# Kernel tuning notes

Measured on AMD Instinct MI355X. Metric: run time of the kernel, lower is better.

The kernel has to match this reference:

```python
import jax, jax.numpy as jnp
import numpy as np

MIN_SIZE = 16.0
PH, PW, SCALE = 7, 7, 0.0625


def _context_anchor(rois, hh, hw):
    """rois: [N,5] (batch_idx,x1,y1,x2,y2). Returns [N*8,5] context boxes, col0 = 0 label."""
    N = rois.shape[0]
    x1, y1, x2, y2 = rois[:, 1], rois[:, 2], rois[:, 3], rois[:, 4]
    w, h = x2 - x1, y2 - y1
    k = jnp.arange(3, dtype=rois.dtype)
    sx = x1[:, None] + w[:, None] * (k - 0.5)  # x1 - w + w*k + w/2
    sy = y1[:, None] + h[:, None] * (k - 0.5)
    # np.meshgrid(shift_x, shift_y).ravel() is y-major
    cx = jnp.broadcast_to(sx[:, None, :], (N, 3, 3)).reshape(N, 9)
    cy = jnp.broadcast_to(sy[:, :, None], (N, 3, 3)).reshape(N, 9)
    boxes = jnp.stack([cx - w[:, None] / 4, cy - h[:, None] / 4,
                       cx + w[:, None] / 4, cy + h[:, None] / 4], -1)  # [N,9,4]
    bw = boxes[..., 2] - boxes[..., 0] + 1
    bh = boxes[..., 3] - boxes[..., 1] + 1
    invalid = ((boxes[..., 0] < 0) | (boxes[..., 1] < 0) |
               (boxes[..., 2] >= hw) | (boxes[..., 3] >= hh) |
               (bw < MIN_SIZE) | (bh < MIN_SIZE))
    boxes = jnp.where(invalid[..., None], rois[:, None, 1:5], boxes)
    boxes = boxes[:, jnp.array([0, 1, 2, 3, 5, 6, 7, 8]), :]  # drop center cell
    gt = boxes.reshape(N * 8, 4)  # K = 8N
    # IoU(all roi boxes, gt) with +1 pixel convention (bbox_overlaps_batch)
    A = rois[:, 1:5]
    aw, ah = A[:, 2] - A[:, 0] + 1, A[:, 3] - A[:, 1] + 1
    gw, gh = gt[:, 2] - gt[:, 0] + 1, gt[:, 3] - gt[:, 1] + 1
    iw = jnp.maximum(jnp.minimum(A[:, None, 2], gt[None, :, 2]) - jnp.maximum(A[:, None, 0], gt[None, :, 0]) + 1, 0)
    ih = jnp.maximum(jnp.minimum(A[:, None, 3], gt[None, :, 3]) - jnp.maximum(A[:, None, 1], gt[None, :, 1]) + 1, 0)
    inter = iw * ih
    ov = inter / ((aw * ah)[:, None] + (gw * gh)[None, :] - inter)  # [N,K]
    ov = jnp.where(((gw == 1) & (gh == 1))[None, :], 0.0, ov)
    ov = jnp.where(((aw == 1) & (ah == 1))[:, None], -1.0, ov)
    gt_max = ov.max(0)          # best overlap per gt box
    best = ov.argmax(0)         # index of best-matching roi (torch's `_`)
    labels = gt_max >= 0.3
    w_cell, h_cell = gt[:, 2] - gt[:, 0], gt[:, 3] - gt[:, 1]
    rw = jnp.where(labels, rois[best, 3] - rois[best, 1], 0.0)
    rh = jnp.where(labels, rois[best, 4] - rois[best, 2], 0.0)
    labels = (labels & ~(jnp.maximum(rw, rh) >= jnp.maximum(w_cell, h_cell))
                     & ~(jnp.minimum(rw, rh) < jnp.minimum(w_cell, h_cell) / 3))
    gt = jnp.where(labels[:, None], rois[best][:, 1:5], gt)
    # original zeroes labels at the end -> label column is all zeros
    return jnp.concatenate([jnp.zeros((N * 8, 1), rois.dtype), gt], -1)


def _roi_pool(features, boxes, ph, pw, scale):
    """Classic Caffe max RoIPool. Assumes batch_size==1 (all batch indices 0)."""
    _, C, H, W = features.shape
    f = features[0]  # [C,H,W]
    sw = jnp.round(boxes[:, 1] * scale)
    sh = jnp.round(boxes[:, 2] * scale)
    ew = jnp.round(boxes[:, 3] * scale)
    eh = jnp.round(boxes[:, 4] * scale)
    bsh = jnp.maximum(eh - sh + 1, 1.0) / ph
    bsw = jnp.maximum(ew - sw + 1, 1.0) / pw
    ii = jnp.arange(ph, dtype=f.dtype)
    jj = jnp.arange(pw, dtype=f.dtype)
    hs = jnp.clip(jnp.floor(ii[None, :] * bsh[:, None]) + sh[:, None], 0, H)   # [R,ph]
    he = jnp.clip(jnp.ceil((ii[None, :] + 1) * bsh[:, None]) + sh[:, None], 0, H)
    ws = jnp.clip(jnp.floor(jj[None, :] * bsw[:, None]) + sw[:, None], 0, W)   # [R,pw]
    we = jnp.clip(jnp.ceil((jj[None, :] + 1) * bsw[:, None]) + sw[:, None], 0, W)
    hidx = jnp.arange(H, dtype=f.dtype)
    widx = jnp.arange(W, dtype=f.dtype)
    mask_h = (hidx >= hs[..., None]) & (hidx < he[..., None])  # [R,ph,H]
    mask_w = (widx >= ws[..., None]) & (widx < we[..., None])  # [R,pw,W]
    NEG = jnp.asarray(-1e30, f.dtype)
    # separable masked max: reduce W per pw-bin, then H per ph-bin
    colmax = jnp.stack([jnp.where(mask_w[:, j, None, None, :], f[None], NEG).max(-1)
                        for j in range(pw)], axis=1)           # [R,pw,C,H]
    out = jnp.stack([jnp.where(mask_h[:, i, None, None, :], colmax, NEG).max(-1)
                     for i in range(ph)], axis=1)              # [R,ph,pw,C]
    valid = mask_h.any(-1)[:, :, None] & mask_w.any(-1)[:, None, :]
    out = jnp.where(valid[..., None], out, 0.0)                # empty bins -> 0
    return jnp.transpose(out, (0, 3, 1, 2))                    # [R,C,ph,pw]


def reference(features, rois, hh, hw):
    N = rois.shape[0]
    gt = _context_anchor(rois, hh, hw).reshape(N, 8, 5)
    cat_rois = jnp.concatenate([rois[:, None, :], gt], 1).reshape(-1, 5)  # [9N,5]
    pool = _roi_pool(features, cat_rois, PH, PW, SCALE)                   # [9N,C,7,7]
    pool_feat = pool.reshape(N, -1, PW, PH)                               # [N,9C,7,7]
    return pool_feat, cat_rois


def setup_inputs() -> dict:
    key = jax.random.key(0)
    k1, k2, k3, k4, k5 = jax.random.split(key, 5)
    N, C, Hf, Wf, IMG = 32, 256, 40, 40, 640
    x1 = jax.random.uniform(k1, (N,), minval=0.0, maxval=IMG - 220.0)
    y1 = jax.random.uniform(k2, (N,), minval=0.0, maxval=IMG - 220.0)
    bw = jax.random.uniform(k3, (N,), minval=80.0, maxval=200.0)
    bh = jax.random.uniform(k4, (N,), minval=80.0, maxval=200.0)
    rois = jnp.stack([jnp.zeros((N,)), x1, y1, x1 + bw, y1 + bh], -1).astype(jnp.float32)
    features = jax.random.normal(k5, (1, C, Hf, Wf), dtype=jnp.float32)
    return {"features": features, "rois": rois, "hh": 640, "hw": 640}
```

## Files before the change

### kernel.cpp

```cpp
#include <hip/hip_runtime.h>
#include <math.h>

#define N_ROIS   32
#define N_CAT    (N_ROIS * 9)
#define C_FEAT   256
#define H_FEAT   40
#define W_FEAT   40
#define P_FEAT   (H_FEAT * W_FEAT)
#define PH       7
#define PW       7
#define SCALE    0.0625f
#define MIN_SIZE 16.0f
#define CELLS    (PH * PW)
#define POOL_PER_BOX (C_FEAT * CELLS)
#define OUT_POOL_ELEMS ((size_t)N_CAT * POOL_PER_BOX)

#define N_TRANS_BLOCKS (P_FEAT / 32 * (C_FEAT / 32))

#define CH_G     64
#define NCHG     4
#define NBLK     (N_CAT * NCHG)
#define TPB      448
#define WROWS    14
#define WCOLS    14
#define PIX      (WROWS * WCOLS)
#define SLOTS    (PIX + 2)
#define WIN_FLTS (SLOTS * CH_G)
#define OBUF_FLTS (CH_G * CELLS)
#define QPP      (CH_G / 4)
#define STAGE_N  (PIX * QPP)

__global__ void prep_kernel(const float* __restrict__ f,
                            const float* __restrict__ rois,
                            const int* __restrict__ hh_p,
                            const int* __restrict__ hw_p,
                            float* __restrict__ ft,
                            float* __restrict__ cat_out,
                            int use_transpose) {
    __shared__ float tile[32][33];
    __shared__ float R[N_ROIS * 5];
    const int bid = blockIdx.x;
    const int tid = threadIdx.x;

    if (bid < N_TRANS_BLOCKS) {
        if (!use_transpose) return;
        const int pt = (bid % (P_FEAT / 32)) * 32;
        const int ct = (bid / (P_FEAT / 32)) * 32;
        const int lx = tid & 31;
        const int ly = tid >> 5;
        #pragma unroll
        for (int i = 0; i < 32; i += 8)
            tile[ly + i][lx] = f[(ct + ly + i) * P_FEAT + (pt + lx)];
        __syncthreads();
        #pragma unroll
        for (int i = 0; i < 32; i += 8)
            ft[(pt + ly + i) * C_FEAT + (ct + lx)] = tile[lx][ly + i];
        return;
    }

    if (tid < N_ROIS * 5) R[tid] = rois[tid];
    __syncthreads();

    const float hh = (float)(*hh_p);
    const float hw = (float)(*hw_p);

    const int g = tid;
    const int n = g >> 3;
    const int j = g & 7;
    const int m = (j < 4) ? j : j + 1;
    const int r  = m / 3;
    const int cc = m % 3;

    const float x1 = R[n * 5 + 1], y1 = R[n * 5 + 2];
    const float x2 = R[n * 5 + 3], y2 = R[n * 5 + 4];
    const float w = x2 - x1, h = y2 - y1;

    const float cx = x1 + w * ((float)cc - 0.5f);
    const float cy = y1 + h * ((float)r  - 0.5f);
    float bx1 = cx - w * 0.25f;
    float by1 = cy - h * 0.25f;
    float bx2 = cx + w * 0.25f;
    float by2 = cy + h * 0.25f;
    const float bw = bx2 - bx1 + 1.0f;
    const float bh = by2 - by1 + 1.0f;
    const bool invalid = (bx1 < 0.0f) || (by1 < 0.0f) ||
                         (bx2 >= hw) || (by2 >= hh) ||
                         (bw < MIN_SIZE) || (bh < MIN_SIZE);
    if (invalid) { bx1 = x1; by1 = y1; bx2 = x2; by2 = y2; }

    const float gw = bx2 - bx1 + 1.0f;
    const float gh = by2 - by1 + 1.0f;
    const float garea = gw * gh;
    const bool gdeg = (gw == 1.0f) && (gh == 1.0f);

    float best_ov = -INFINITY;
    int best = 0;
    for (int a = 0; a < N_ROIS; ++a) {
        const float ax1 = R[a * 5 + 1], ay1 = R[a * 5 + 2];
        const float ax2 = R[a * 5 + 3], ay2 = R[a * 5 + 4];
        const float aw = ax2 - ax1 + 1.0f, ah = ay2 - ay1 + 1.0f;
        float iw = fminf(ax2, bx2) - fmaxf(ax1, bx1) + 1.0f;
        float ih = fminf(ay2, by2) - fmaxf(ay1, by1) + 1.0f;
        iw = fmaxf(iw, 0.0f);
        ih = fmaxf(ih, 0.0f);
        const float inter = iw * ih;
        float ov = inter / (aw * ah + garea - inter);
        if (gdeg) ov = 0.0f;
        if (aw == 1.0f && ah == 1.0f) ov = -1.0f;
        if (ov > best_ov) { best_ov = ov; best = a; }
    }

    bool label = (best_ov >= 0.3f);
    const float w_cell = bx2 - bx1;
    const float h_cell = by2 - by1;
    const float rw = label ? (R[best * 5 + 3] - R[best * 5 + 1]) : 0.0f;
    const float rh = label ? (R[best * 5 + 4] - R[best * 5 + 2]) : 0.0f;
    label = label &&
            !(fmaxf(rw, rh) >= fmaxf(w_cell, h_cell)) &&
            !(fminf(rw, rh) < fminf(w_cell, h_cell) / 3.0f);
    if (label) {
        bx1 = R[best * 5 + 1]; by1 = R[best * 5 + 2];
        bx2 = R[best * 5 + 3]; by2 = R[best * 5 + 4];
    }

    float* row = cat_out + (size_t)(n * 9 + 1 + j) * 5;
    row[0] = 0.0f;
    row[1] = bx1; row[2] = by1; row[3] = bx2; row[4] = by2;
    if (j == 0) {
        float* rr = cat_out + (size_t)(n * 9) * 5;
        #pragma unroll
        for (int t = 0; t < 5; ++t) rr[t] = R[n * 5 + t];
    }
}

__global__ __launch_bounds__(TPB) void
pool_v8(const float* __restrict__ ft,
        const float* __restrict__ cat_rois,
        float* __restrict__ out) {
    __shared__ __align__(16) float win[WIN_FLTS];

    const int s   = (blockIdx.x & 7) * (NBLK / 8) + (blockIdx.x >> 3);
    const int b   = s >> 2;
    const int cg  = s & 3;
    const int tid = threadIdx.x;
    const int cl  = tid & 63;
    const int i   = tid >> 6;

    const float* cr = cat_rois + (size_t)b * 5;
    const float bx1 = cr[1], by1 = cr[2], bx2 = cr[3], by2 = cr[4];
    const float sw = rintf(bx1 * SCALE);
    const float sh = rintf(by1 * SCALE);
    const float ew = rintf(bx2 * SCALE);
    const float eh = rintf(by2 * SCALE);
    const float bsh = fmaxf(eh - sh + 1.0f, 1.0f) * (1.0f / (float)PH);
    const float bsw = fmaxf(ew - sw + 1.0f, 1.0f) * (1.0f / (float)PW);

    const int hs = __builtin_amdgcn_readfirstlane(
        (int)fminf(fmaxf(floorf((float)i * bsh) + sh, 0.0f), (float)H_FEAT));
    const int he = __builtin_amdgcn_readfirstlane(
        (int)fminf(fmaxf(ceilf((float)(i + 1) * bsh) + sh, 0.0f), (float)H_FEAT));

    int ws[PW], we[PW];
    #pragma unroll
    for (int j = 0; j < PW; ++j) {
        ws[j] = __builtin_amdgcn_readfirstlane(
            (int)fminf(fmaxf(floorf((float)j * bsw) + sw, 0.0f), (float)W_FEAT));
        we[j] = __builtin_amdgcn_readfirstlane(
            (int)fminf(fmaxf(ceilf((float)(j + 1) * bsw) + sw, 0.0f), (float)W_FEAT));
    }
    const int xs = ws[0];
    const int ys = __builtin_amdgcn_readfirstlane(
        (int)fminf(fmaxf(sh, 0.0f), (float)H_FEAT));

    const bool narrow = (bsw <= 2.0f) && (bsh <= 2.0f);
    const bool rowv = (he > hs);

    if (narrow) {
        const float* fb = ft + cg * CH_G;
        #pragma unroll
        for (int t = 0; t < STAGE_N / TPB; ++t) {
            const int e = tid + t * TPB;
            const int q = e & (QPP - 1);
            const int p = e >> 4;
            const int py = p / WCOLS;
            const int px = p - py * WCOLS;
            const int gy = (ys + py < H_FEAT - 1) ? (ys + py) : (H_FEAT - 1);
            const int gx = (xs + px < W_FEAT - 1) ? (xs + px) : (W_FEAT - 1);
            const float4 v = *(const float4*)(fb + ((size_t)(gy * W_FEAT + gx)
                                                    << 8) + (q << 2));
            *(float4*)(win + p * CH_G + q * 4) = v;
        }
        __syncthreads();

        float mx[PW];
        #pragma unroll
        for (int j = 0; j < PW; ++j) mx[j] = -1e30f;

        int off[PW], nj[PW];
        #pragma unroll
        for (int j = 0; j < PW; ++j) {
            off[j] = ws[j] - xs;
            nj[j]  = we[j] - ws[j];
        }
        for (int y = hs; y < he; ++y) {
            const float* wr = win + (y - ys) * (WCOLS * CH_G) + cl;
            #pragma unroll
            for (int j = 0; j < PW; ++j) {
                const float* p0 = wr + off[j] * CH_G;
                const float d0 = p0[0];
                const float d1 = p0[CH_G];
                const float d2 = p0[2 * CH_G];
                if (nj[j] > 0) mx[j] = fmaxf(mx[j], d0);
                if (nj[j] > 1) mx[j] = fmaxf(mx[j], d1);
                if (nj[j] > 2) mx[j] = fmaxf(mx[j], d2);
            }
        }
        __syncthreads();

        float* orow = win + cl * CELLS + i * PW;
        #pragma unroll
        for (int j = 0; j < PW; ++j)
            orow[j] = (rowv && (nj[j] > 0)) ? mx[j] : 0.0f;
        __syncthreads();

        const float4* src = (const float4*)win;
        float4* dst = (float4*)(out + (size_t)b * POOL_PER_BOX
                                    + (size_t)cg * OBUF_FLTS);
        dst[tid] = src[tid];
        const int e2 = tid + TPB;
        if (e2 < OBUF_FLTS / 4) dst[e2] = src[e2];
    } else {
        const int c = cg * CH_G + cl;
        float mx[PW];
        #pragma unroll
        for (int j = 0; j < PW; ++j) mx[j] = -1e30f;
        for (int y = hs; y < he; ++y) {
            #pragma unroll
            for (int j = 0; j < PW; ++j)
                for (int x = ws[j]; x < we[j]; ++x)
                    mx[j] = fmaxf(mx[j], ft[(size_t)(y * W_FEAT + x) * C_FEAT + c]);
        }
        float* ob = out + (size_t)b * POOL_PER_BOX + (size_t)c * CELLS + i * PW;
        #pragma unroll
        for (int j = 0; j < PW; ++j)
            ob[j] = (rowv && (we[j] > ws[j])) ? mx[j] : 0.0f;
    }
}

__global__ __launch_bounds__(256) void
roi_pool_kernel_nchw(const float* __restrict__ feat,
                     const float* __restrict__ cat_rois,
                     float* __restrict__ out) {
    const int i = blockIdx.x / N_CAT;
    const int b = blockIdx.x % N_CAT;
    const int c = threadIdx.x;

    const float* cr = cat_rois + (size_t)b * 5;
    const float sw = rintf(cr[1] * SCALE);
    const float sh = rintf(cr[2] * SCALE);
    const float ew = rintf(cr[3] * SCALE);
    const float eh = rintf(cr[4] * SCALE);
    const float bsh = fmaxf(eh - sh + 1.0f, 1.0f) * (1.0f / (float)PH);
    const float bsw = fmaxf(ew - sw + 1.0f, 1.0f) * (1.0f / (float)PW);

    const int hs = (int)fminf(fmaxf(floorf((float)i * bsh) + sh, 0.0f), (float)H_FEAT);
    const int he = (int)fminf(fmaxf(ceilf((float)(i + 1) * bsh) + sh, 0.0f), (float)H_FEAT);
    int ws[PW], we[PW];
    #pragma unroll
    for (int j = 0; j < PW; ++j) {
        ws[j] = (int)fminf(fmaxf(floorf((float)j * bsw) + sw, 0.0f), (float)W_FEAT);
        we[j] = (int)fminf(fmaxf(ceilf((float)(j + 1) * bsw) + sw, 0.0f), (float)W_FEAT);
    }
    float mx[PW];
    #pragma unroll
    for (int j = 0; j < PW; ++j) mx[j] = -1e30f;
    for (int y = hs; y < he; ++y) {
        const float* fr = feat + (size_t)c * P_FEAT + y * W_FEAT;
        #pragma unroll
        for (int j = 0; j < PW; ++j)
            for (int x = ws[j]; x < we[j]; ++x)
                mx[j] = fmaxf(mx[j], fr[x]);
    }
    const bool rowv = (he > hs);
    float* ob = out + (size_t)b * POOL_PER_BOX + (size_t)c * CELLS + i * PW;
    #pragma unroll
    for (int j = 0; j < PW; ++j)
        ob[j] = (rowv && (we[j] > ws[j])) ? mx[j] : 0.0f;
}

extern "C" void kernel_launch(void* const* d_in, const int* in_sizes, int n_in,
                              void* d_out, int out_size, void* d_ws, size_t ws_size,
                              hipStream_t stream) {
    const float* features = (const float*)d_in[0];
    const float* rois     = (const float*)d_in[1];
    const int*   hh_p     = (const int*)d_in[2];
    const int*   hw_p     = (const int*)d_in[3];

    float* out      = (float*)d_out;
    float* cat_out  = out + OUT_POOL_ELEMS;
    float* ft       = (float*)d_ws;

    const size_t ft_bytes = (size_t)C_FEAT * P_FEAT * sizeof(float);
    const int use_transpose = (ws_size >= ft_bytes) ? 1 : 0;

    hipLaunchKernelGGL(prep_kernel, dim3(N_TRANS_BLOCKS + 1), dim3(256), 0, stream,
                       features, rois, hh_p, hw_p, ft, cat_out, use_transpose);

    if (use_transpose) {
        hipLaunchKernelGGL(pool_v8, dim3(NBLK), dim3(TPB), 0, stream,
                           ft, cat_out, out);
    } else {
        hipLaunchKernelGGL(roi_pool_kernel_nchw, dim3(PH * N_CAT), dim3(C_FEAT), 0, stream,
                           features, cat_out, out);
    }
}
```

Measured before the change: 79.59 us.

## Fuse prep and pooling into one cooperative kernel with atomic work queue

```diff
diff --git a/kernel.cpp b/kernel.cpp
--- a/kernel.cpp
+++ b/kernel.cpp
@@ -1,4 +1,5 @@
 #include <hip/hip_runtime.h>
+#include <hip/hip_cooperative_groups.h>
 #include <math.h>
 
 #define N_ROIS   32
@@ -19,7 +20,8 @@
 
 #define CH_G     64
 #define NCHG     4
-#define NBLK     (N_CAT * NCHG)
+#define NUNIT    (N_CAT * NCHG)
+#define NBLK8    1152
 #define TPB      448
 #define WROWS    14
 #define WCOLS    14
@@ -28,7 +30,246 @@
 #define WIN_FLTS (SLOTS * CH_G)
 #define OBUF_FLTS (CH_G * CELLS)
 #define QPP      (CH_G / 4)
-#define STAGE_N  (PIX * QPP)
+
+#define CBLK     384
+
+__global__ __launch_bounds__(TPB, 4) void
+coop_v9(const float* __restrict__ f,
+        const float* __restrict__ rois,
+        const int* __restrict__ hh_p,
+        const int* __restrict__ hw_p,
+        float* __restrict__ out,
+        float* __restrict__ ft) {
+    __shared__ __align__(16) float win[WIN_FLTS];
+    __shared__ unsigned su;
+
+    const int bid = blockIdx.x;
+    const int tid = threadIdx.x;
+    unsigned* ctr = (unsigned*)(ft + (size_t)C_FEAT * P_FEAT);
+    float* cat_out = out + OUT_POOL_ELEMS;
+
+    if (bid == 0 && tid == 0) atomicExch(ctr, 0u);
+
+    float (*tile)[33] = (float(*)[33])win;
+    #pragma unroll
+    for (int pass = 0; pass < 2; ++pass) {
+        const int tno = bid + pass * CBLK;
+        const bool act = (tno < N_TRANS_BLOCKS) && (pass == 0 || bid < N_TRANS_BLOCKS - CBLK);
+        if (!act) continue;
+        const int pt = (tno % (P_FEAT / 32)) * 32;
+        const int ct = (tno / (P_FEAT / 32)) * 32;
+        const int lx = tid & 31;
+        const int ly = (tid >> 5) & 7;
+        if (tid < 256) {
+            #pragma unroll
+            for (int ii = 0; ii < 32; ii += 8)
+                tile[ly + ii][lx] = f[(ct + ly + ii) * P_FEAT + (pt + lx)];
+        }
+        __syncthreads();
+        if (tid < 256) {
+            #pragma unroll
+            for (int ii = 0; ii < 32; ii += 8)
+                ft[(pt + ly + ii) * C_FEAT + (ct + lx)] = tile[lx][ly + ii];
+        }
+        __syncthreads();
+    }
+
+    if (bid == CBLK - 1) {
+        float* R = win;
+        if (tid < N_ROIS * 5) R[tid] = rois[tid];
+        __syncthreads();
+        if (tid < 256) {
+            const float hh = (float)(*hh_p);
+            const float hw = (float)(*hw_p);
+            const int g = tid;
+            const int n = g >> 3;
+            const int j = g & 7;
+            const int m = (j < 4) ? j : j + 1;
+            const int r  = m / 3;
+            const int cc = m % 3;
+
+            const float x1 = R[n * 5 + 1], y1 = R[n * 5 + 2];
+            const float x2 = R[n * 5 + 3], y2 = R[n * 5 + 4];
+            const float w = x2 - x1, h = y2 - y1;
+
+            const float cx = x1 + w * ((float)cc - 0.5f);
+            const float cy = y1 + h * ((float)r  - 0.5f);
+            float bx1 = cx - w * 0.25f;
+            float by1 = cy - h * 0.25f;
+            float bx2 = cx + w * 0.25f;
+            float by2 = cy + h * 0.25f;
+            const float bw = bx2 - bx1 + 1.0f;
+            const float bh = by2 - by1 + 1.0f;
+            const bool invalid = (bx1 < 0.0f) || (by1 < 0.0f) ||
+                                 (bx2 >= hw) || (by2 >= hh) ||
+                                 (bw < MIN_SIZE) || (bh < MIN_SIZE);
+            if (invalid) { bx1 = x1; by1 = y1; bx2 = x2; by2 = y2; }
+
+            const float gw = bx2 - bx1 + 1.0f;
+            const float gh = by2 - by1 + 1.0f;
+            const float garea = gw * gh;
+            const bool gdeg = (gw == 1.0f) && (gh == 1.0f);
+
+            float best_ov = -INFINITY;
+            int best = 0;
+            for (int a = 0; a < N_ROIS; ++a) {
+                const float ax1 = R[a * 5 + 1], ay1 = R[a * 5 + 2];
+                const float ax2 = R[a * 5 + 3], ay2 = R[a * 5 + 4];
+                const float aw = ax2 - ax1 + 1.0f, ah = ay2 - ay1 + 1.0f;
+                float iw = fminf(ax2, bx2) - fmaxf(ax1, bx1) + 1.0f;
+                float ih = fminf(ay2, by2) - fmaxf(ay1, by1) + 1.0f;
+                iw = fmaxf(iw, 0.0f);
+                ih = fmaxf(ih, 0.0f);
+                const float inter = iw * ih;
+                float ov = inter / (aw * ah + garea - inter);
+                if (gdeg) ov = 0.0f;
+                if (aw == 1.0f && ah == 1.0f) ov = -1.0f;
+                if (ov > best_ov) { best_ov = ov; best = a; }
+            }
+
+            bool label = (best_ov >= 0.3f);
+            const float w_cell = bx2 - bx1;
+            const float h_cell = by2 - by1;
+            const float rw = label ? (R[best * 5 + 3] - R[best * 5 + 1]) : 0.0f;
+            const float rh = label ? (R[best * 5 + 4] - R[best * 5 + 2]) : 0.0f;
+            label = label &&
+                    !(fmaxf(rw, rh) >= fmaxf(w_cell, h_cell)) &&
+                    !(fminf(rw, rh) < fminf(w_cell, h_cell) / 3.0f);
+            if (label) {
+                bx1 = R[best * 5 + 1]; by1 = R[best * 5 + 2];
+                bx2 = R[best * 5 + 3]; by2 = R[best * 5 + 4];
+            }
+
+            float* row = cat_out + (size_t)(n * 9 + 1 + j) * 5;
+            row[0] = 0.0f;
+            row[1] = bx1; row[2] = by1; row[3] = bx2; row[4] = by2;
+            if (j == 0) {
+                float* rr = cat_out + (size_t)(n * 9) * 5;
+                #pragma unroll
+                for (int t = 0; t < 5; ++t) rr[t] = R[n * 5 + t];
+            }
+        }
+        __syncthreads();
+    }
+
+    cooperative_groups::this_grid().sync();
+
+    const int cl = tid & 63;
+    const int i  = tid >> 6;
+
+    for (;;) {
+        if (tid == 0) su = atomicAdd(ctr, 1u);
+        __syncthreads();
+        const unsigned u = su;
+        if (u >= (unsigned)NUNIT) break;
+
+        const int b  = (int)(u >> 2);
+        const int cg = (int)(u & 3);
+
+        const float* cr = cat_out + (size_t)b * 5;
+        const float bx1 = cr[1], by1 = cr[2], bx2 = cr[3], by2 = cr[4];
+        const float sw = rintf(bx1 * SCALE);
+        const float sh = rintf(by1 * SCALE);
+        const float ew = rintf(bx2 * SCALE);
+        const float eh = rintf(by2 * SCALE);
+        const float bsh = fmaxf(eh - sh + 1.0f, 1.0f) * (1.0f / (float)PH);
+        const float bsw = fmaxf(ew - sw + 1.0f, 1.0f) * (1.0f / (float)PW);
+
+        const int hs = __builtin_amdgcn_readfirstlane(
+            (int)fminf(fmaxf(floorf((float)i * bsh) + sh, 0.0f), (float)H_FEAT));
+        const int he = __builtin_amdgcn_readfirstlane(
+            (int)fminf(fmaxf(ceilf((float)(i + 1) * bsh) + sh, 0.0f), (float)H_FEAT));
+
+        int ws[PW], we[PW];
+        #pragma unroll
+        for (int j = 0; j < PW; ++j) {
+            ws[j] = __builtin_amdgcn_readfirstlane(
+                (int)fminf(fmaxf(floorf((float)j * bsw) + sw, 0.0f), (float)W_FEAT));
+            we[j] = __builtin_amdgcn_readfirstlane(
+                (int)fminf(fmaxf(ceilf((float)(j + 1) * bsw) + sw, 0.0f), (float)W_FEAT));
+        }
+        const int xs = ws[0];
+        const int ys = __builtin_amdgcn_readfirstlane(
+            (int)fminf(fmaxf(sh, 0.0f), (float)H_FEAT));
+        const int yend = __builtin_amdgcn_readfirstlane(
+            (int)fminf(fmaxf(ceilf((float)PH * bsh) + sh, 0.0f), (float)H_FEAT));
+        const int WH = yend - ys;
+
+        const bool narrow = (bsw <= 2.0f) && (bsh <= 2.0f);
+        const bool rowv = (he > hs);
+
+        if (narrow) {
+            const float* fb = ft + cg * CH_G;
+            const int nq4 = WH * WCOLS * QPP;
+            for (int e = tid; e < nq4; e += TPB) {
+                const int q = e & (QPP - 1);
+                const int p = e >> 4;
+                const int py = p / WCOLS;
+                const int px = p - py * WCOLS;
+                const int gy = (ys + py < H_FEAT - 1) ? (ys + py) : (H_FEAT - 1);
+                const int gx = (xs + px < W_FEAT - 1) ? (xs + px) : (W_FEAT - 1);
+                const float4 v = *(const float4*)(fb + ((size_t)(gy * W_FEAT + gx)
+                                                        << 8) + (q << 2));
+                *(float4*)(win + p * CH_G + q * 4) = v;
+            }
+            __syncthreads();
+
+            float mx[PW];
+            #pragma unroll
+            for (int j = 0; j < PW; ++j) mx[j] = -1e30f;
+
+            int off[PW], nj[PW];
+            #pragma unroll
+            for (int j = 0; j < PW; ++j) {
+                off[j] = ws[j] - xs;
+                nj[j]  = we[j] - ws[j];
+            }
+            for (int y = hs; y < he; ++y) {
+                const float* wr = win + (y - ys) * (WCOLS * CH_G) + cl;
+                #pragma unroll
+                for (int j = 0; j < PW; ++j) {
+                    const float* p0 = wr + off[j] * CH_G;
+                    const float d0 = p0[0];
+                    const float d1 = p0[CH_G];
+                    const float d2 = p0[2 * CH_G];
+                    if (nj[j] > 0) mx[j] = fmaxf(mx[j], d0);
+                    if (nj[j] > 1) mx[j] = fmaxf(mx[j], d1);
+                    if (nj[j] > 2) mx[j] = fmaxf(mx[j], d2);
+                }
+            }
+            __syncthreads();
+
+            float* orow = win + cl * CELLS + i * PW;
+            #pragma unroll
+            for (int j = 0; j < PW; ++j)
+                orow[j] = (rowv && (nj[j] > 0)) ? mx[j] : 0.0f;
+            __syncthreads();
+
+            const float4* src = (const float4*)win;
+            float4* dst = (float4*)(out + (size_t)b * POOL_PER_BOX
+                                        + (size_t)cg * OBUF_FLTS);
+            dst[tid] = src[tid];
+            const int e2 = tid + TPB;
+            if (e2 < OBUF_FLTS / 4) dst[e2] = src[e2];
+        } else {
+            const int c = cg * CH_G + cl;
+            float mx[PW];
+            #pragma unroll
+            for (int j = 0; j < PW; ++j) mx[j] = -1e30f;
+            for (int y = hs; y < he; ++y) {
+                #pragma unroll
+                for (int j = 0; j < PW; ++j)
+                    for (int x = ws[j]; x < we[j]; ++x)
+                        mx[j] = fmaxf(mx[j], ft[(size_t)(y * W_FEAT + x) * C_FEAT + c]);
+            }
+            float* ob = out + (size_t)b * POOL_PER_BOX + (size_t)c * CELLS + i * PW;
+            #pragma unroll
+            for (int j = 0; j < PW; ++j)
+                ob[j] = (rowv && (we[j] > ws[j])) ? mx[j] : 0.0f;
+        }
+        __syncthreads();
+    }
+}
 
 __global__ void prep_kernel(const float* __restrict__ f,
                             const float* __restrict__ rois,
@@ -63,7 +304,6 @@
 
     const float hh = (float)(*hh_p);
     const float hw = (float)(*hw_p);
-
     const int g = tid;
     const int n = g >> 3;
     const int j = g & 7;
@@ -139,7 +379,7 @@
         float* __restrict__ out) {
     __shared__ __align__(16) float win[WIN_FLTS];
 
-    const int s   = (blockIdx.x & 7) * (NBLK / 8) + (blockIdx.x >> 3);
+    const int s   = (blockIdx.x & 7) * (NBLK8 / 8) + (blockIdx.x >> 3);
     const int b   = s >> 2;
     const int cg  = s & 3;
     const int tid = threadIdx.x;
@@ -178,7 +418,7 @@
     if (narrow) {
         const float* fb = ft + cg * CH_G;
         #pragma unroll
-        for (int t = 0; t < STAGE_N / TPB; ++t) {
+        for (int t = 0; t < (PIX * QPP) / TPB; ++t) {
             const int e = tid + t * TPB;
             const int q = e & (QPP - 1);
             const int p = e >> 4;
@@ -301,16 +541,24 @@
     float* ft       = (float*)d_ws;
 
     const size_t ft_bytes = (size_t)C_FEAT * P_FEAT * sizeof(float);
-    const int use_transpose = (ws_size >= ft_bytes) ? 1 : 0;
-
-    hipLaunchKernelGGL(prep_kernel, dim3(N_TRANS_BLOCKS + 1), dim3(256), 0, stream,
-                       features, rois, hh_p, hw_p, ft, cat_out, use_transpose);
+    const int use_transpose = (ws_size >= ft_bytes + 64) ? 1 : 0;
 
     if (use_transpose) {
-        hipLaunchKernelGGL(pool_v8, dim3(NBLK), dim3(TPB), 0, stream,
+        void* args[] = {(void*)&features, (void*)&rois, (void*)&hh_p,
+                        (void*)&hw_p, (void*)&out, (void*)&ft};
+        hipError_t e = hipLaunchCooperativeKernel((const void*)coop_v9,
+                                                  dim3(CBLK), dim3(TPB),
+                                                  args, 0, stream);
+        if (e == hipSuccess) return;
+        (void)hipGetLastError();
+        hipLaunchKernelGGL(prep_kernel, dim3(N_TRANS_BLOCKS + 1), dim3(256), 0,
+                           stream, features, rois, hh_p, hw_p, ft, cat_out, 1);
+        hipLaunchKernelGGL(pool_v8, dim3(NBLK8), dim3(TPB), 0, stream,
                            ft, cat_out, out);
     } else {
-        hipLaunchKernelGGL(roi_pool_kernel_nchw, dim3(PH * N_CAT), dim3(C_FEAT), 0, stream,
-                           features, cat_out, out);
+        hipLaunchKernelGGL(prep_kernel, dim3(N_TRANS_BLOCKS + 1), dim3(256), 0,
+                           stream, features, rois, hh_p, hw_p, ft, cat_out, 0);
+        hipLaunchKernelGGL(roi_pool_kernel_nchw, dim3(PH * N_CAT), dim3(C_FEAT),
+                           0, stream, features, cat_out, out);
     }
 }
```

New measurement: 127.2 us. 1.6x slower.
